# Performance work log

Hardware: AMD Instinct MI355X
Metric: run time of the kernel (lower is better)

## Reference

```python
import jax, jax.numpy as jnp
import numpy as np

B, S, D, H, NL = 4, 1024, 512, 8, 2
DFF = 4 * D
EPS = 1e-5


def _layernorm(x, g, b):
    m = x.mean(-1, keepdims=True)
    v = ((x - m) ** 2).mean(-1, keepdims=True)
    return (x - m) / jnp.sqrt(v + EPS) * g + b


def _forward(x, Wq, bq, Wk, bk, Wv, bv, Wo, bo, W1, b1, W2, b2, ln1_g, ln1_b, ln2_g, ln2_b):
    Bn, Sn, Dn = x.shape
    Nl, Hh = Wq.shape[0], Wq.shape[1]
    dk = Dn // Hh  # scaling uses dmodel//h even though heads are full-width (faithful to SDPA)
    for i in range(Nl):
        # per-head full-width projections: each head maps dmodel -> dmodel
        q = jnp.einsum('bsd,hed->bhse', x, Wq[i]) + bq[i][:, None, :]
        k = jnp.einsum('bsd,hed->bhse', x, Wk[i]) + bk[i][:, None, :]
        v = jnp.einsum('bsd,hed->bhse', x, Wv[i]) + bv[i][:, None, :]
        scores = jnp.einsum('bhse,bhte->bhst', q, k) / jnp.sqrt(jnp.asarray(dk, x.dtype))
        attn = jax.nn.softmax(scores, axis=-1)
        heads = jnp.einsum('bhst,bhte->bhse', attn, v)          # [B,H,S,D]
        cat = heads.transpose(0, 2, 1, 3).reshape(Bn, Sn, Hh * Dn)  # concat heads -> [B,S,H*D]
        mha_out = cat @ Wo[i].T + bo[i]
        x = _layernorm(x + mha_out, ln1_g[i], ln1_b[i])
        ff = jax.nn.relu(x @ W1[i].T + b1[i]) @ W2[i].T + b2[i]
        x = _layernorm(x + ff, ln2_g[i], ln2_b[i])
    return x


def setup_inputs() -> dict:
    key = jax.random.key(0)
    ks = jax.random.split(key, 12)
    def w(k, shape, fan_in):
        return (jax.random.normal(k, shape, jnp.float32) / np.sqrt(fan_in)).astype(jnp.float32)
    inp = {
        'x': jax.random.normal(ks[0], (B, S, D), jnp.float32),
        'Wq': w(ks[1], (NL, H, D, D), D), 'bq': jnp.zeros((NL, H, D), jnp.float32),
        'Wk': w(ks[2], (NL, H, D, D), D), 'bk': jnp.zeros((NL, H, D), jnp.float32),
        'Wv': w(ks[3], (NL, H, D, D), D), 'bv': jnp.zeros((NL, H, D), jnp.float32),
        'Wo': w(ks[4], (NL, D, H * D), H * D), 'bo': jnp.zeros((NL, D), jnp.float32),
        'W1': w(ks[5], (NL, DFF, D), D), 'b1': jnp.zeros((NL, DFF), jnp.float32),
        'W2': w(ks[6], (NL, D, DFF), DFF), 'b2': jnp.zeros((NL, D), jnp.float32),
        'ln1_g': jnp.ones((NL, D), jnp.float32), 'ln1_b': jnp.zeros((NL, D), jnp.float32),
        'ln2_g': jnp.ones((NL, D), jnp.float32), 'ln2_b': jnp.zeros((NL, D), jnp.float32),
    }
    return inp


def reference(x, Wq, bq, Wk, bk, Wv, bv, Wo, bo, W1, b1, W2, b2, ln1_g, ln1_b, ln2_g, ln2_b):
    return _forward(x, Wq, bq, Wk, bk, Wv, bv, Wo, bo, W1, b1, W2, b2, ln1_g, ln1_b, ln2_g, ln2_b)
```

## Files before the change

### kernel.cpp

```cpp
#include <hip/hip_runtime.h>
#include <cstdint>
#include <cstddef>

#define NB 4
#define NS 1024
#define ND 512
#define NH 8
#define NLAYER 2
#define NDFF 2048

typedef __attribute__((ext_vector_type(8))) short short8;
typedef __attribute__((ext_vector_type(4))) float f32x4;
typedef __attribute__((ext_vector_type(4))) unsigned short u16x4;
typedef unsigned short u16;
typedef long long ll;

__device__ __forceinline__ float b2f(u16 u) {
  union { unsigned int i; float f; } x; x.i = ((unsigned int)u) << 16; return x.f;
}
__device__ __forceinline__ u16 f2b(float f) {
  union { float f; unsigned int i; } x; x.f = f;
  return (u16)((x.i + 0x7FFF + ((x.i >> 16) & 1)) >> 16);
}

struct Zm { int div; ll hi, lo; };
__device__ __forceinline__ ll zoff(Zm m, int z) {
  return (ll)(z / m.div) * m.hi + (ll)(z % m.div) * m.lo;
}

enum { F_BF16 = 1, F_RELU = 2, F_BCOL = 4, F_BROW = 8, F_RESID = 16 };

__device__ __forceinline__ void load_lds16(const void* g, void* s) {
  __builtin_amdgcn_global_load_lds(
      (const __attribute__((address_space(1))) void*)(uintptr_t)g,
      (__attribute__((address_space(3))) void*)(uint32_t)(uintptr_t)s, 16, 0, 0);
}

__global__ void __launch_bounds__(256)
gemm_bt(const u16* __restrict__ A, int lda, Zm za,
        const u16* __restrict__ Bw, int ldb, Zm zb,
        const u16* __restrict__ Bw2, const float* __restrict__ bias2, int zsplit,
        void* __restrict__ Cv, int ldc, Zm zc,
        const float* __restrict__ bias, Zm zbias,
        const float* __restrict__ resid,
        float scale, int K, int flags)
{
  __shared__ __align__(16) char smem[2][16384];

  const int gx = gridDim.x, gy = gridDim.y;
  int id = (blockIdx.z * gy + blockIdx.y) * gx + blockIdx.x;
  const int nwg = gx * gy * (int)gridDim.z;
  if ((nwg & 7) == 0) id = (id & 7) * (nwg >> 3) + (id >> 3);
  const int bx = id % gx;
  const int rest = id / gx;
  const int by = rest % gy;
  const int z0 = rest / gy;

  int zB = z0;
  const u16* Bsel = Bw;
  const float* bsel = bias;
  if (z0 >= zsplit) { Bsel = Bw2; bsel = bias2; zB = z0 - zsplit; }

  A    += zoff(za, z0);
  Bsel += zoff(zb, zB);

  const int bm = by * 128, bn = bx * 128;
  const int t = threadIdx.x;
  const int w = t >> 6, lane = t & 63;
  const int wr = w >> 1, wc = w & 1;

  const u16* ga0 = A    + (size_t)(bm + (t >> 2)) * lda + ((t & 3) << 3);
  const u16* ga1 = ga0 + (size_t)64 * lda;
  const u16* gb0 = Bsel + (size_t)(bn + (t >> 2)) * ldb + ((t & 3) << 3);
  const u16* gb1 = gb0 + (size_t)64 * ldb;

  auto STAGE = [&](int sel, int kt) {
    const int k0 = kt << 5;
    char* sa = smem[sel] + (w << 10);
    char* sb = smem[sel] + 8192 + (w << 10);
    load_lds16(ga0 + k0, sa);
    load_lds16(ga1 + k0, sa + 4096);
    load_lds16(gb0 + k0, sb);
    load_lds16(gb1 + k0, sb + 4096);
  };

  f32x4 acc[4][4];
#pragma unroll
  for (int i = 0; i < 4; ++i)
#pragma unroll
    for (int j = 0; j < 4; ++j) acc[i][j] = (f32x4){0.f, 0.f, 0.f, 0.f};

  const int fr = lane & 15;
  const int kg = (lane >> 4) << 3;

  const int nt = K >> 5;
  STAGE(0, 0);
  __syncthreads();
  int cur = 0;
  for (int kt = 0; kt < nt; ++kt) {
    if (kt + 1 < nt) STAGE(cur ^ 1, kt + 1);
    const u16* la = (const u16*)smem[cur];
    const u16* lb = (const u16*)(smem[cur] + 8192);
    short8 af[4], bf[4];
#pragma unroll
    for (int mi = 0; mi < 4; ++mi)
      af[mi] = *(const short8*)(la + (wr * 64 + mi * 16 + fr) * 32 + kg);
#pragma unroll
    for (int ni = 0; ni < 4; ++ni)
      bf[ni] = *(const short8*)(lb + (wc * 64 + ni * 16 + fr) * 32 + kg);
#pragma unroll
    for (int mi = 0; mi < 4; ++mi)
#pragma unroll
      for (int ni = 0; ni < 4; ++ni)
        asm volatile("v_mfma_f32_16x16x32_bf16 %0, %1, %2, %0"
                     : "+v"(acc[mi][ni]) : "v"(af[mi]), "v"(bf[ni]));
    __syncthreads();
    cur ^= 1;
  }

  asm volatile("s_nop 7\n\ts_nop 7" ::: "memory");

  const ll co = zoff(zc, z0);
  const float* bz = (flags & (F_BCOL | F_BROW)) ? bsel + zoff(zbias, zB) : nullptr;
  const int r0 = (lane >> 4) << 2;
  const int c0 = lane & 15;
#pragma unroll
  for (int mi = 0; mi < 4; ++mi) {
#pragma unroll
    for (int ni = 0; ni < 4; ++ni) {
#pragma unroll
      for (int r = 0; r < 4; ++r) {
        const int grow = bm + wr * 64 + mi * 16 + r0 + r;
        const int gcol = bn + wc * 64 + ni * 16 + c0;
        float v = acc[mi][ni][r] * scale;
        if (flags & F_BCOL) v += bz[gcol];
        if (flags & F_BROW) v += bz[grow];
        if (flags & F_RELU) v = fmaxf(v, 0.f);
        if (flags & F_RESID) v += resid[(size_t)grow * ldc + gcol];
        const ll idx = co + (ll)grow * ldc + gcol;
        if (flags & F_BF16) ((u16*)Cv)[idx] = f2b(v);
        else                ((float*)Cv)[idx] = v;
      }
    }
  }
}

__global__ void __launch_bounds__(256)
softmax_rows(u16* __restrict__ sc)
{
  const int t = threadIdx.x, w = t >> 6, lane = t & 63;
  u16* p = sc + ((ll)blockIdx.x * 4 + w) * 1024 + lane * 16;
  short8 a = *(const short8*)p;
  short8 b = *(const short8*)(p + 8);
  float v[16];
#pragma unroll
  for (int j = 0; j < 8; ++j) { v[j] = b2f((u16)a[j]); v[8 + j] = b2f((u16)b[j]); }
  float mx = v[0];
#pragma unroll
  for (int j = 1; j < 16; ++j) mx = fmaxf(mx, v[j]);
#pragma unroll
  for (int o = 32; o >= 1; o >>= 1) mx = fmaxf(mx, __shfl_xor(mx, o));
  float s = 0.f;
#pragma unroll
  for (int j = 0; j < 16; ++j) { v[j] = __expf(v[j] - mx); s += v[j]; }
#pragma unroll
  for (int o = 32; o >= 1; o >>= 1) s += __shfl_xor(s, o);
  const float inv = 1.f / s;
  short8 oa, ob;
#pragma unroll
  for (int j = 0; j < 8; ++j) {
    oa[j] = (short)f2b(v[j] * inv);
    ob[j] = (short)f2b(v[8 + j] * inv);
  }
  *(short8*)p = oa;
  *(short8*)(p + 8) = ob;
}

__global__ void __launch_bounds__(256)
ln_red(const float* __restrict__ parts, int np, ll pstride,
       const float* __restrict__ bias, const float* __restrict__ resid,
       const float* __restrict__ g, const float* __restrict__ be,
       float* __restrict__ xout, u16* __restrict__ xbout)
{
  const int t = threadIdx.x, w = t >> 6, lane = t & 63;
  const ll row = (ll)blockIdx.x * 4 + w;
  const ll base = row * ND + lane * 8;
  float v[8];
  *(f32x4*)(v)     = *(const f32x4*)(resid + base);
  *(f32x4*)(v + 4) = *(const f32x4*)(resid + base + 4);
#pragma unroll
  for (int j = 0; j < 8; ++j) v[j] += bias[lane * 8 + j];
  for (int pIdx = 0; pIdx < np; ++pIdx) {
    const float* pp = parts + pIdx * pstride + base;
    f32x4 a0 = *(const f32x4*)(pp);
    f32x4 a1 = *(const f32x4*)(pp + 4);
    v[0] += a0.x; v[1] += a0.y; v[2] += a0.z; v[3] += a0.w;
    v[4] += a1.x; v[5] += a1.y; v[6] += a1.z; v[7] += a1.w;
  }
  float s = 0.f, q = 0.f;
#pragma unroll
  for (int j = 0; j < 8; ++j) { s += v[j]; q += v[j] * v[j]; }
#pragma unroll
  for (int o = 32; o >= 1; o >>= 1) { s += __shfl_xor(s, o); q += __shfl_xor(q, o); }
  const float mean = s * (1.f / ND);
  const float var  = q * (1.f / ND) - mean * mean;
  const float inv  = 1.f / sqrtf(var + 1e-5f);
#pragma unroll
  for (int j = 0; j < 8; ++j) {
    const int c = lane * 8 + j;
    const float y = (v[j] - mean) * inv * g[c] + be[c];
    xout[row * ND + c] = y;
    xbout[row * ND + c] = f2b(y);
  }
}

struct CvtJobs { const float* src[7]; u16* dst[7]; ll n[7]; };

__global__ void __launch_bounds__(256)
cvt7(CvtJobs j)
{
  const int z = blockIdx.y;
  const ll i = ((ll)blockIdx.x * 256 + threadIdx.x) * 4;
  if (i >= j.n[z]) return;
  f32x4 v = *(const f32x4*)(j.src[z] + i);
  u16x4 o;
  o.x = f2b(v.x); o.y = f2b(v.y); o.z = f2b(v.z); o.w = f2b(v.w);
  *(u16x4*)(j.dst[z] + i) = o;
}

extern "C" void kernel_launch(void* const* d_in, const int* in_sizes, int n_in,
                              void* d_out, int out_size, void* d_ws, size_t ws_size,
                              hipStream_t stream)
{
  (void)in_sizes; (void)n_in; (void)out_size; (void)ws_size;
  const float* x_in = (const float*)d_in[0];
  const float* Wq = (const float*)d_in[1];  const float* bq = (const float*)d_in[2];
  const float* Wk = (const float*)d_in[3];  const float* bk = (const float*)d_in[4];
  const float* Wv = (const float*)d_in[5];  const float* bv = (const float*)d_in[6];
  const float* Wo = (const float*)d_in[7];  const float* bo = (const float*)d_in[8];
  const float* W1 = (const float*)d_in[9];  const float* b1 = (const float*)d_in[10];
  const float* W2 = (const float*)d_in[11]; const float* b2 = (const float*)d_in[12];
  const float* ln1g = (const float*)d_in[13]; const float* ln1b = (const float*)d_in[14];
  const float* ln2g = (const float*)d_in[15]; const float* ln2b = (const float*)d_in[16];

  char* p = (char*)d_ws;
  auto alloc = [&](ll bytes) { char* r = p; p += (bytes + 255) & ~(ll)255; return r; };
  const ll nWq = (ll)NLAYER * NH * ND * ND;
  const ll nWo = (ll)NLAYER * ND * NH * ND;
  const ll nW1 = (ll)NLAYER * NDFF * ND;
  const ll nX  = (ll)NB * NS * ND;

  u16* wq_b = (u16*)alloc(nWq * 2);
  u16* wk_b = (u16*)alloc(nWq * 2);
  u16* wv_b = (u16*)alloc(nWq * 2);
  u16* wo_b = (u16*)alloc(nWo * 2);
  u16* w1_b = (u16*)alloc(nW1 * 2);
  u16* w2_b = (u16*)alloc(nW1 * 2);
  u16* xb   = (u16*)alloc(nX * 2);
  u16* qb   = (u16*)alloc((ll)NH * NB * NS * ND * 2);
  u16* kb   = (u16*)alloc((ll)NH * NB * NS * ND * 2);
  u16* vT   = (u16*)alloc((ll)NH * NB * ND * NS * 2);
  u16* scb  = (u16*)alloc((ll)NB * NH * NS * NS * 2);
  u16* cat = kb;
  u16* ffh = qb;
  float* parts = (float*)scb;

  CvtJobs cj;
  cj.src[0] = Wq; cj.dst[0] = wq_b; cj.n[0] = nWq;
  cj.src[1] = Wk; cj.dst[1] = wk_b; cj.n[1] = nWq;
  cj.src[2] = Wv; cj.dst[2] = wv_b; cj.n[2] = nWq;
  cj.src[3] = Wo; cj.dst[3] = wo_b; cj.n[3] = nWo;
  cj.src[4] = W1; cj.dst[4] = w1_b; cj.n[4] = nW1;
  cj.src[5] = W2; cj.dst[5] = w2_b; cj.n[5] = nW1;
  cj.src[6] = x_in; cj.dst[6] = xb; cj.n[6] = nX;
  cvt7<<<dim3((unsigned)((nWq / 4 + 255) / 256), 7), 256, 0, stream>>>(cj);

  float* xf = (float*)d_out;
  const Zm Z0{1, 0, 0};
  const ll PSTR = (ll)NB * NS * ND;
  const int ZINF = 1 << 30;

  for (int i = 0; i < NLAYER; ++i) {
    const float* resid1 = (i == 0) ? x_in : xf;
    const ll woff = (ll)i * NH * ND * ND;

    gemm_bt<<<dim3(ND/128, (NB*NS)/128, 2*NH), 256, 0, stream>>>(
        xb, ND, Z0,
        wq_b + woff, ND, Zm{1, (ll)ND * ND, 0},
        wk_b + woff, bk + (ll)i * NH * ND, NH,
        qb, ND, Zm{1, (ll)NB * NS * ND, 0},
        bq + (ll)i * NH * ND, Zm{1, ND, 0}, nullptr, 1.f, ND, F_BF16 | F_BCOL);

    gemm_bt<<<dim3(NS/128, ND/128, NH*NB), 256, 0, stream>>>(
        wv_b + woff, ND, Zm{NB, (ll)ND * ND, 0},
        xb, ND, Zm{NB, 0, (ll)NS * ND},
        xb, nullptr, ZINF,
        vT, NS, Zm{1, (ll)ND * NS, 0},
        bv + (ll)i * NH * ND, Zm{NB, ND, 0}, nullptr, 1.f, ND, F_BF16 | F_BROW);

    gemm_bt<<<dim3(NS/128, NS/128, NH*NB), 256, 0, stream>>>(
        qb, ND, Zm{NB, (ll)NB * NS * ND, (ll)NS * ND},
        kb, ND, Zm{NB, (ll)NB * NS * ND, (ll)NS * ND},
        kb, nullptr, ZINF,
        scb, NS, Zm{1, (ll)NS * NS, 0},
        nullptr, Z0, nullptr, 0.125f, ND, F_BF16);

    softmax_rows<<<dim3(NB * NH * NS / 4), 256, 0, stream>>>(scb);

    gemm_bt<<<dim3(ND/128, NS/128, NH*NB), 256, 0, stream>>>(
        scb, NS, Zm{1, (ll)NS * NS, 0},
        vT, NS, Zm{1, (ll)ND * NS, 0},
        vT, nullptr, ZINF,
        cat, NH * ND, Zm{NB, (ll)ND, (ll)NS * NH * ND},
        nullptr, Z0, nullptr, 1.f, NS, F_BF16);

    gemm_bt<<<dim3(ND/128, (NB*NS)/128, 8), 256, 0, stream>>>(
        cat, NH * ND, Zm{1, 512, 0},
        wo_b + (ll)i * ND * NH * ND, NH * ND, Zm{1, 512, 0},
        wo_b, nullptr, ZINF,
        parts, ND, Zm{1, PSTR, 0},
        nullptr, Z0, nullptr, 1.f, 512, 0);

    ln_red<<<dim3(NB * NS / 4), 256, 0, stream>>>(
        parts, 8, PSTR, bo + (ll)i * ND, resid1,
        ln1g + (ll)i * ND, ln1b + (ll)i * ND, xf, xb);

    gemm_bt<<<dim3(NDFF/128, (NB*NS)/128, 1), 256, 0, stream>>>(
        xb, ND, Z0,
        w1_b + (ll)i * NDFF * ND, ND, Z0,
        w1_b, nullptr, ZINF,
        ffh, NDFF, Z0,
        b1 + (ll)i * NDFF, Z0, nullptr, 1.f, ND, F_BF16 | F_BCOL | F_RELU);

    gemm_bt<<<dim3(ND/128, (NB*NS)/128, 4), 256, 0, stream>>>(
        ffh, NDFF, Zm{1, 512, 0},
        w2_b + (ll)i * ND * NDFF, NDFF, Zm{1, 512, 0},
        w2_b, nullptr, ZINF,
        parts, ND, Zm{1, PSTR, 0},
        nullptr, Z0, nullptr, 1.f, 512, 0);

    ln_red<<<dim3(NB * NS / 4), 256, 0, stream>>>(
        parts, 4, PSTR, b2 + (ll)i * ND, xf,
        ln2g + (ll)i * ND, ln2b + (ll)i * ND, xf, xb);
  }
}
```

Baseline: 681.6 us.

## Replace 128x128 GEMM with 256x256 tile 8-wave kernel using swizzled LDS

Replaces the 4-wave 128x128x32 GEMM with an 8-wave kernel using 256x256 output tiles, a K step of 64 and a 64 KB-per-stage double buffer. LDS rows are XOR-swizzled to avoid bank conflicts. The next stage's A and B loads are issued between MFMA groups, and s_setprio is raised around the MFMAs. The larger tile is meant to cut global and LDS traffic per FLOP and hide load latency. The W2 split-K changes from 4 to 8 slices to keep enough blocks, at the cost of much higher LDS use per block, fewer blocks per CU, and an extra partial sum to reduce.

```diff
diff --git a/kernel.cpp b/kernel.cpp
--- a/kernel.cpp
+++ b/kernel.cpp
@@ -36,16 +36,19 @@
       (__attribute__((address_space(3))) void*)(uint32_t)(uintptr_t)s, 16, 0, 0);
 }
 
-__global__ void __launch_bounds__(256)
-gemm_bt(const u16* __restrict__ A, int lda, Zm za,
-        const u16* __restrict__ Bw, int ldb, Zm zb,
-        const u16* __restrict__ Bw2, const float* __restrict__ bias2, int zsplit,
-        void* __restrict__ Cv, int ldc, Zm zc,
-        const float* __restrict__ bias, Zm zbias,
-        const float* __restrict__ resid,
-        float scale, int K, int flags)
-{
-  __shared__ __align__(16) char smem[2][16384];
+#define MFMA16(d, a, b) \
+  asm volatile("v_mfma_f32_16x16x32_bf16 %0, %1, %2, %0" : "+v"(d) : "v"(a), "v"(b))
+
+__global__ void __launch_bounds__(512, 2)
+gemm8(const u16* __restrict__ A, int lda, Zm za,
+      const u16* __restrict__ Bw, int ldb, Zm zb,
+      const u16* __restrict__ Bw2, const float* __restrict__ bias2, int zsplit,
+      void* __restrict__ Cv, int ldc, Zm zc,
+      const float* __restrict__ bias, Zm zbias,
+      const float* __restrict__ resid,
+      float scale, int K, int flags)
+{
+  __shared__ __align__(16) char smem[2][65536];
 
   const int gx = gridDim.x, gy = gridDim.y;
   int id = (blockIdx.z * gy + blockIdx.y) * gx + blockIdx.x;
@@ -64,58 +67,92 @@
   A    += zoff(za, z0);
   Bsel += zoff(zb, zB);
 
-  const int bm = by * 128, bn = bx * 128;
+  const int bm = by * 256, bn = bx * 256;
   const int t = threadIdx.x;
   const int w = t >> 6, lane = t & 63;
-  const int wr = w >> 1, wc = w & 1;
-
-  const u16* ga0 = A    + (size_t)(bm + (t >> 2)) * lda + ((t & 3) << 3);
-  const u16* ga1 = ga0 + (size_t)64 * lda;
-  const u16* gb0 = Bsel + (size_t)(bn + (t >> 2)) * ldb + ((t & 3) << 3);
-  const u16* gb1 = gb0 + (size_t)64 * ldb;
-
-  auto STAGE = [&](int sel, int kt) {
-    const int k0 = kt << 5;
-    char* sa = smem[sel] + (w << 10);
-    char* sb = smem[sel] + 8192 + (w << 10);
-    load_lds16(ga0 + k0, sa);
-    load_lds16(ga1 + k0, sa + 4096);
-    load_lds16(gb0 + k0, sb);
-    load_lds16(gb1 + k0, sb + 4096);
+  const int wr = w >> 2, wc = w & 3;
+
+  const int swcol = (((t & 7) ^ ((t >> 3) & 7)) << 3);
+  const u16* srcA = A    + (size_t)(bm + (t >> 3)) * lda + swcol;
+  const u16* srcB = Bsel + (size_t)(bn + (t >> 3)) * ldb + swcol;
+  char* const sbase = (char*)smem;
+  const int wofs = w << 10;
+
+  auto STAGE_A = [&](int kt) {
+    const ll kofs = (ll)kt << 6;
+    char* d0 = sbase + ((kt & 1) << 16);
+#pragma unroll
+    for (int h = 0; h < 2; ++h)
+#pragma unroll
+      for (int i = 0; i < 2; ++i)
+        load_lds16(srcA + (size_t)(h * 128 + i * 64) * lda + kofs,
+                   d0 + h * 16384 + i * 8192 + wofs);
   };
-
-  f32x4 acc[4][4];
-#pragma unroll
-  for (int i = 0; i < 4; ++i)
+  auto STAGE_B = [&](int kt) {
+    const ll kofs = (ll)kt << 6;
+    char* d0 = sbase + ((kt & 1) << 16) + 32768;
+#pragma unroll
+    for (int h = 0; h < 2; ++h)
+#pragma unroll
+      for (int i = 0; i < 2; ++i)
+        load_lds16(srcB + (size_t)(h * 128 + i * 64) * ldb + kofs,
+                   d0 + h * 16384 + i * 8192 + wofs);
+  };
+
+  const int fr  = lane & 15;
+  const int khi = lane >> 4;
+  const int swz = (fr & 7) << 3;
+  const int colk0 = (khi * 8) ^ swz;
+  const int colk1 = (32 + khi * 8) ^ swz;
+  const int bbase = (wc & 1) * 64;
+
+  f32x4 acc[8][4];
+#pragma unroll
+  for (int i = 0; i < 8; ++i)
 #pragma unroll
     for (int j = 0; j < 4; ++j) acc[i][j] = (f32x4){0.f, 0.f, 0.f, 0.f};
 
-  const int fr = lane & 15;
-  const int kg = (lane >> 4) << 3;
-
-  const int nt = K >> 5;
-  STAGE(0, 0);
+  const int nt = K >> 6;
+  STAGE_A(0);
+  STAGE_B(0);
   __syncthreads();
-  int cur = 0;
-  for (int kt = 0; kt < nt; ++kt) {
-    if (kt + 1 < nt) STAGE(cur ^ 1, kt + 1);
-    const u16* la = (const u16*)smem[cur];
-    const u16* lb = (const u16*)(smem[cur] + 8192);
-    short8 af[4], bf[4];
-#pragma unroll
-    for (int mi = 0; mi < 4; ++mi)
-      af[mi] = *(const short8*)(la + (wr * 64 + mi * 16 + fr) * 32 + kg);
-#pragma unroll
-    for (int ni = 0; ni < 4; ++ni)
-      bf[ni] = *(const short8*)(lb + (wc * 64 + ni * 16 + fr) * 32 + kg);
-#pragma unroll
-    for (int mi = 0; mi < 4; ++mi)
-#pragma unroll
-      for (int ni = 0; ni < 4; ++ni)
-        asm volatile("v_mfma_f32_16x16x32_bf16 %0, %1, %2, %0"
-                     : "+v"(acc[mi][ni]) : "v"(af[mi]), "v"(bf[ni]));
+
+  for (int T = 0; T < nt; ++T) {
+    const char* bufp = sbase + ((T & 1) << 16);
+    const u16* sA = (const u16*)(bufp + wr * 16384);
+    const u16* sB = (const u16*)(bufp + 32768 + (wc >> 1) * 16384);
+    const bool more = (T + 1) < nt;
+
+    short8 bfr[4][2];
+#pragma unroll
+    for (int ni = 0; ni < 4; ++ni) {
+      const int rb = (bbase + ni * 16 + fr) * 64;
+      bfr[ni][0] = *(const short8*)(sB + rb + colk0);
+      bfr[ni][1] = *(const short8*)(sB + rb + colk1);
+    }
+
+#pragma unroll
+    for (int q = 0; q < 4; ++q) {
+      short8 afr[2][2];
+#pragma unroll
+      for (int sub = 0; sub < 2; ++sub) {
+        const int ra = (q * 32 + sub * 16 + fr) * 64;
+        afr[sub][0] = *(const short8*)(sA + ra + colk0);
+        afr[sub][1] = *(const short8*)(sA + ra + colk1);
+      }
+      if (q == 0 && more) STAGE_A(T + 1);
+      if (q == 1 && more) STAGE_B(T + 1);
+      __builtin_amdgcn_s_setprio(1);
+#pragma unroll
+      for (int sub = 0; sub < 2; ++sub)
+#pragma unroll
+        for (int ni = 0; ni < 4; ++ni) {
+          MFMA16(acc[q * 2 + sub][ni], afr[sub][0], bfr[ni][0]);
+          MFMA16(acc[q * 2 + sub][ni], afr[sub][1], bfr[ni][1]);
+        }
+      __builtin_amdgcn_s_setprio(0);
+    }
     __syncthreads();
-    cur ^= 1;
   }
 
   asm volatile("s_nop 7\n\ts_nop 7" ::: "memory");
@@ -125,12 +162,12 @@
   const int r0 = (lane >> 4) << 2;
   const int c0 = lane & 15;
 #pragma unroll
-  for (int mi = 0; mi < 4; ++mi) {
+  for (int mi = 0; mi < 8; ++mi) {
 #pragma unroll
     for (int ni = 0; ni < 4; ++ni) {
 #pragma unroll
       for (int r = 0; r < 4; ++r) {
-        const int grow = bm + wr * 64 + mi * 16 + r0 + r;
+        const int grow = bm + wr * 128 + mi * 16 + r0 + r;
         const int gcol = bn + wc * 64 + ni * 16 + c0;
         float v = acc[mi][ni][r] * scale;
         if (flags & F_BCOL) v += bz[gcol];
@@ -284,21 +321,21 @@
     const float* resid1 = (i == 0) ? x_in : xf;
     const ll woff = (ll)i * NH * ND * ND;
 
-    gemm_bt<<<dim3(ND/128, (NB*NS)/128, 2*NH), 256, 0, stream>>>(
+    gemm8<<<dim3(ND/256, (NB*NS)/256, 2*NH), 512, 0, stream>>>(
         xb, ND, Z0,
         wq_b + woff, ND, Zm{1, (ll)ND * ND, 0},
         wk_b + woff, bk + (ll)i * NH * ND, NH,
         qb, ND, Zm{1, (ll)NB * NS * ND, 0},
         bq + (ll)i * NH * ND, Zm{1, ND, 0}, nullptr, 1.f, ND, F_BF16 | F_BCOL);
 
-    gemm_bt<<<dim3(NS/128, ND/128, NH*NB), 256, 0, stream>>>(
+    gemm8<<<dim3(NS/256, ND/256, NH*NB), 512, 0, stream>>>(
         wv_b + woff, ND, Zm{NB, (ll)ND * ND, 0},
         xb, ND, Zm{NB, 0, (ll)NS * ND},
         xb, nullptr, ZINF,
         vT, NS, Zm{1, (ll)ND * NS, 0},
         bv + (ll)i * NH * ND, Zm{NB, ND, 0}, nullptr, 1.f, ND, F_BF16 | F_BROW);
 
-    gemm_bt<<<dim3(NS/128, NS/128, NH*NB), 256, 0, stream>>>(
+    gemm8<<<dim3(NS/256, NS/256, NH*NB), 512, 0, stream>>>(
         qb, ND, Zm{NB, (ll)NB * NS * ND, (ll)NS * ND},
         kb, ND, Zm{NB, (ll)NB * NS * ND, (ll)NS * ND},
         kb, nullptr, ZINF,
@@ -307,14 +344,14 @@
 
     softmax_rows<<<dim3(NB * NH * NS / 4), 256, 0, stream>>>(scb);
 
-    gemm_bt<<<dim3(ND/128, NS/128, NH*NB), 256, 0, stream>>>(
+    gemm8<<<dim3(ND/256, NS/256, NH*NB), 512, 0, stream>>>(
         scb, NS, Zm{1, (ll)NS * NS, 0},
         vT, NS, Zm{1, (ll)ND * NS, 0},
         vT, nullptr, ZINF,
         cat, NH * ND, Zm{NB, (ll)ND, (ll)NS * NH * ND},
         nullptr, Z0, nullptr, 1.f, NS, F_BF16);
 
-    gemm_bt<<<dim3(ND/128, (NB*NS)/128, 8), 256, 0, stream>>>(
+    gemm8<<<dim3(ND/256, (NB*NS)/256, 8), 512, 0, stream>>>(
         cat, NH * ND, Zm{1, 512, 0},
         wo_b + (ll)i * ND * NH * ND, NH * ND, Zm{1, 512, 0},
         wo_b, nullptr, ZINF,
@@ -325,22 +362,22 @@
         parts, 8, PSTR, bo + (ll)i * ND, resid1,
         ln1g + (ll)i * ND, ln1b + (ll)i * ND, xf, xb);
 
-    gemm_bt<<<dim3(NDFF/128, (NB*NS)/128, 1), 256, 0, stream>>>(
+    gemm8<<<dim3(NDFF/256, (NB*NS)/256, 1), 512, 0, stream>>>(
         xb, ND, Z0,
         w1_b + (ll)i * NDFF * ND, ND, Z0,
         w1_b, nullptr, ZINF,
         ffh, NDFF, Z0,
         b1 + (ll)i * NDFF, Z0, nullptr, 1.f, ND, F_BF16 | F_BCOL | F_RELU);
 
-    gemm_bt<<<dim3(ND/128, (NB*NS)/128, 4), 256, 0, stream>>>(
-        ffh, NDFF, Zm{1, 512, 0},
-        w2_b + (ll)i * ND * NDFF, NDFF, Zm{1, 512, 0},
+    gemm8<<<dim3(ND/256, (NB*NS)/256, 8), 512, 0, stream>>>(
+        ffh, NDFF, Zm{1, 256, 0},
+        w2_b + (ll)i * ND * NDFF, NDFF, Zm{1, 256, 0},
         w2_b, nullptr, ZINF,
         parts, ND, Zm{1, PSTR, 0},
-        nullptr, Z0, nullptr, 1.f, 512, 0);
+        nullptr, Z0, nullptr, 1.f, 256, 0);
 
     ln_red<<<dim3(NB * NS / 4), 256, 0, stream>>>(
-        parts, 4, PSTR, b2 + (ll)i * ND, xf,
+        parts, 8, PSTR, b2 + (ll)i * ND, xf,
         ln2g + (ll)i * ND, ln2b + (ll)i * ND, xf, xb);
   }
 }
```

Result: slower. 754.4 us (+10.7%).

## Fuse QK^T, softmax and PV into a flash-attention kernel

Applied to the files above, without the earlier changes.

Replaces the separate score GEMM, row softmax and PV GEMM with one fused kernel that keeps scores in registers and LDS and applies an online softmax over 128-key tiles. This avoids writing and rereading the bf16 score matrix in global memory and removes two launches. The output-projection split-K is also changed from 8 to 4 partitions, and the workspace aliasing is moved so cat and parts share the score buffer. In exchange, Q is reloaded for every KV tile and d-chunk, and the kernel holds a large accumulator array in registers, which may limit occupancy.

```diff
diff --git a/kernel.cpp b/kernel.cpp
--- a/kernel.cpp
+++ b/kernel.cpp
@@ -35,6 +35,9 @@
       (const __attribute__((address_space(1))) void*)(uintptr_t)g,
       (__attribute__((address_space(3))) void*)(uint32_t)(uintptr_t)s, 16, 0, 0);
 }
+
+#define MFMA16(d, a, b) \
+  asm volatile("v_mfma_f32_16x16x32_bf16 %0, %1, %2, %0" : "+v"(d) : "v"(a), "v"(b))
 
 __global__ void __launch_bounds__(256)
 gemm_bt(const u16* __restrict__ A, int lda, Zm za,
@@ -112,8 +115,7 @@
     for (int mi = 0; mi < 4; ++mi)
 #pragma unroll
       for (int ni = 0; ni < 4; ++ni)
-        asm volatile("v_mfma_f32_16x16x32_bf16 %0, %1, %2, %0"
-                     : "+v"(acc[mi][ni]) : "v"(af[mi]), "v"(bf[ni]));
+        MFMA16(acc[mi][ni], af[mi], bf[ni]);
     __syncthreads();
     cur ^= 1;
   }
@@ -145,35 +147,135 @@
   }
 }
 
-__global__ void __launch_bounds__(256)
-softmax_rows(u16* __restrict__ sc)
+__global__ void __launch_bounds__(256, 2)
+fattn(const u16* __restrict__ qg, const u16* __restrict__ kg,
+      const u16* __restrict__ vtg, u16* __restrict__ cat)
 {
-  const int t = threadIdx.x, w = t >> 6, lane = t & 63;
-  u16* p = sc + ((ll)blockIdx.x * 4 + w) * 1024 + lane * 16;
-  short8 a = *(const short8*)p;
-  short8 b = *(const short8*)(p + 8);
-  float v[16];
-#pragma unroll
-  for (int j = 0; j < 8; ++j) { v[j] = b2f((u16)a[j]); v[8 + j] = b2f((u16)b[j]); }
-  float mx = v[0];
-#pragma unroll
-  for (int j = 1; j < 16; ++j) mx = fmaxf(mx, v[j]);
-#pragma unroll
-  for (int o = 32; o >= 1; o >>= 1) mx = fmaxf(mx, __shfl_xor(mx, o));
-  float s = 0.f;
-#pragma unroll
-  for (int j = 0; j < 16; ++j) { v[j] = __expf(v[j] - mx); s += v[j]; }
-#pragma unroll
-  for (int o = 32; o >= 1; o >>= 1) s += __shfl_xor(s, o);
-  const float inv = 1.f / s;
-  short8 oa, ob;
-#pragma unroll
-  for (int j = 0; j < 8; ++j) {
-    oa[j] = (short)f2b(v[j] * inv);
-    ob[j] = (short)f2b(v[8 + j] * inv);
-  }
-  *(short8*)p = oa;
-  *(short8*)(p + 8) = ob;
+  __shared__ __align__(16) u16 qk_lds[192 * 128];
+  __shared__ __align__(16) u16 p_lds[64 * 136];
+
+  int id = blockIdx.x;
+  id = (id & 7) * 64 + (id >> 3);
+  const int qt = id & 15;
+  const int hb = id >> 4;
+  const int h = hb >> 2, b = hb & 3;
+
+  const ll hbase = (ll)h * NB * NS * ND;
+  const u16* Q  = qg  + hbase + ((ll)(b * NS + qt * 64)) * ND;
+  const u16* Kp = kg  + hbase + (ll)b * NS * ND;
+  const u16* VT = vtg + (ll)hb * ND * NS;
+  u16* Op = cat + ((ll)(b * NS + qt * 64)) * (NH * ND) + h * ND;
+
+  const int t = threadIdx.x;
+  const int w = t >> 6, lane = t & 63;
+  const int fr = lane & 15, khi = lane >> 4;
+
+  const int srow = t >> 4;
+  const int scol = (((t & 15) ^ (srow & 7)) << 3);
+  char* const qkb = (char*)qk_lds;
+  const int wslab = w << 10;
+
+  f32x4 o[4][8];
+#pragma unroll
+  for (int ec = 0; ec < 4; ++ec)
+#pragma unroll
+    for (int nf = 0; nf < 8; ++nf) o[ec][nf] = (f32x4){0.f, 0.f, 0.f, 0.f};
+  float m_r[4] = {-1e30f, -1e30f, -1e30f, -1e30f};
+  float l_r[4] = {0.f, 0.f, 0.f, 0.f};
+
+  for (int kv = 0; kv < 8; ++kv) {
+    f32x4 s[8];
+#pragma unroll
+    for (int nf = 0; nf < 8; ++nf) s[nf] = (f32x4){0.f, 0.f, 0.f, 0.f};
+
+    for (int dch = 0; dch < 4; ++dch) {
+#pragma unroll
+      for (int i = 0; i < 4; ++i)
+        load_lds16(Q + (ll)(i * 16 + srow) * ND + dch * 128 + scol,
+                   qkb + i * 4096 + wslab);
+#pragma unroll
+      for (int i = 0; i < 8; ++i)
+        load_lds16(Kp + (ll)(kv * 128 + i * 16 + srow) * ND + dch * 128 + scol,
+                   qkb + 16384 + i * 4096 + wslab);
+      __syncthreads();
+#pragma unroll
+      for (int ks = 0; ks < 4; ++ks) {
+        const int gq = (((4 * ks + khi) ^ (fr & 7)) << 3);
+        short8 aq = *(const short8*)(qk_lds + (w * 16 + fr) * 128 + gq);
+#pragma unroll
+        for (int nf = 0; nf < 8; ++nf) {
+          short8 bk = *(const short8*)(qk_lds + 8192 + (nf * 16 + fr) * 128 + gq);
+          MFMA16(s[nf], aq, bk);
+        }
+      }
+      __syncthreads();
+    }
+    asm volatile("s_nop 7\n\ts_nop 7" ::: "memory");
+
+#pragma unroll
+    for (int r = 0; r < 4; ++r) {
+      float v[8];
+#pragma unroll
+      for (int nf = 0; nf < 8; ++nf) v[nf] = s[nf][r] * 0.125f;
+      float mx = v[0];
+#pragma unroll
+      for (int nf = 1; nf < 8; ++nf) mx = fmaxf(mx, v[nf]);
+      mx = fmaxf(mx, __shfl_xor(mx, 1));
+      mx = fmaxf(mx, __shfl_xor(mx, 2));
+      mx = fmaxf(mx, __shfl_xor(mx, 4));
+      mx = fmaxf(mx, __shfl_xor(mx, 8));
+      const float mn = fmaxf(m_r[r], mx);
+      const float f = __expf(m_r[r] - mn);
+      m_r[r] = mn;
+      float sum = 0.f;
+#pragma unroll
+      for (int nf = 0; nf < 8; ++nf) { v[nf] = __expf(v[nf] - mn); sum += v[nf]; }
+      sum += __shfl_xor(sum, 1);
+      sum += __shfl_xor(sum, 2);
+      sum += __shfl_xor(sum, 4);
+      sum += __shfl_xor(sum, 8);
+      l_r[r] = l_r[r] * f + sum;
+#pragma unroll
+      for (int nf = 0; nf < 8; ++nf)
+        p_lds[(w * 16 + 4 * khi + r) * 136 + nf * 16 + fr] = f2b(v[nf]);
+#pragma unroll
+      for (int ec = 0; ec < 4; ++ec)
+#pragma unroll
+        for (int nf = 0; nf < 8; ++nf) o[ec][nf][r] *= f;
+    }
+
+#pragma unroll
+    for (int ec = 0; ec < 4; ++ec) {
+#pragma unroll
+      for (int i = 0; i < 8; ++i)
+        load_lds16(VT + (ll)(ec * 128 + i * 16 + srow) * NS + kv * 128 + scol,
+                   qkb + i * 4096 + wslab);
+      __syncthreads();
+#pragma unroll
+      for (int ks = 0; ks < 4; ++ks) {
+        short8 ap = *(const short8*)(p_lds + (w * 16 + fr) * 136 + 32 * ks + 8 * khi);
+        const int gv = (((4 * ks + khi) ^ (fr & 7)) << 3);
+#pragma unroll
+        for (int nf = 0; nf < 8; ++nf) {
+          short8 bv8 = *(const short8*)(qk_lds + (nf * 16 + fr) * 128 + gv);
+          MFMA16(o[ec][nf], ap, bv8);
+        }
+      }
+      __syncthreads();
+    }
+  }
+
+  asm volatile("s_nop 7\n\ts_nop 7" ::: "memory");
+#pragma unroll
+  for (int r = 0; r < 4; ++r) {
+    const float inv = 1.f / l_r[r];
+    const ll row = (ll)(w * 16 + 4 * khi + r) * (NH * ND);
+#pragma unroll
+    for (int ec = 0; ec < 4; ++ec)
+#pragma unroll
+      for (int nf = 0; nf < 8; ++nf)
+        Op[row + ec * 128 + nf * 16 + fr] = f2b(o[ec][nf][r] * inv);
+  }
 }
 
 __global__ void __launch_bounds__(256)
@@ -261,9 +363,9 @@
   u16* kb   = (u16*)alloc((ll)NH * NB * NS * ND * 2);
   u16* vT   = (u16*)alloc((ll)NH * NB * ND * NS * 2);
   u16* scb  = (u16*)alloc((ll)NB * NH * NS * NS * 2);
-  u16* cat = kb;
+  u16* cat = scb;
+  float* parts = (float*)(scb + (ll)NB * NS * NH * ND);
   u16* ffh = qb;
-  float* parts = (float*)scb;
 
   CvtJobs cj;
   cj.src[0] = Wq; cj.dst[0] = wq_b; cj.n[0] = nWq;
@@ -277,7 +379,7 @@
 
   float* xf = (float*)d_out;
   const Zm Z0{1, 0, 0};
-  const ll PSTR = (ll)NB * NS * ND;
+  const ll PSTR = nX;
   const int ZINF = 1 << 30;
 
   for (int i = 0; i < NLAYER; ++i) {
@@ -298,31 +400,17 @@
         vT, NS, Zm{1, (ll)ND * NS, 0},
         bv + (ll)i * NH * ND, Zm{NB, ND, 0}, nullptr, 1.f, ND, F_BF16 | F_BROW);
 
-    gemm_bt<<<dim3(NS/128, NS/128, NH*NB), 256, 0, stream>>>(
-        qb, ND, Zm{NB, (ll)NB * NS * ND, (ll)NS * ND},
-        kb, ND, Zm{NB, (ll)NB * NS * ND, (ll)NS * ND},
-        kb, nullptr, ZINF,
-        scb, NS, Zm{1, (ll)NS * NS, 0},
-        nullptr, Z0, nullptr, 0.125f, ND, F_BF16);
-
-    softmax_rows<<<dim3(NB * NH * NS / 4), 256, 0, stream>>>(scb);
-
-    gemm_bt<<<dim3(ND/128, NS/128, NH*NB), 256, 0, stream>>>(
-        scb, NS, Zm{1, (ll)NS * NS, 0},
-        vT, NS, Zm{1, (ll)ND * NS, 0},
-        vT, nullptr, ZINF,
-        cat, NH * ND, Zm{NB, (ll)ND, (ll)NS * NH * ND},
-        nullptr, Z0, nullptr, 1.f, NS, F_BF16);
-
-    gemm_bt<<<dim3(ND/128, (NB*NS)/128, 8), 256, 0, stream>>>(
-        cat, NH * ND, Zm{1, 512, 0},
-        wo_b + (ll)i * ND * NH * ND, NH * ND, Zm{1, 512, 0},
+    fattn<<<dim3(512), 256, 0, stream>>>(qb, kb, vT, cat);
+
+    gemm_bt<<<dim3(ND/128, (NB*NS)/128, 4), 256, 0, stream>>>(
+        cat, NH * ND, Zm{1, 1024, 0},
+        wo_b + (ll)i * ND * NH * ND, NH * ND, Zm{1, 1024, 0},
         wo_b, nullptr, ZINF,
         parts, ND, Zm{1, PSTR, 0},
-        nullptr, Z0, nullptr, 1.f, 512, 0);
+        nullptr, Z0, nullptr, 1.f, 1024, 0);
 
     ln_red<<<dim3(NB * NS / 4), 256, 0, stream>>>(
-        parts, 8, PSTR, bo + (ll)i * ND, resid1,
+        parts, 4, PSTR, bo + (ll)i * ND, resid1,
         ln1g + (ll)i * ND, ln1b + (ll)i * ND, xf, xb);
 
     gemm_bt<<<dim3(NDFF/128, (NB*NS)/128, 1), 256, 0, stream>>>(
```

After: 685.0 us. About the same (+0.5%).
